# Kernel tuning notes

Measured on AMD Instinct MI355X. Metric: run time of the kernel, lower is better.

Reference implementation:

```python
import jax, jax.numpy as jnp
import numpy as np

N_DST = 100_000
N_SRC = 200_000
DEG = 16            # fixed avg degree -> E = N_DST*DEG
E = N_DST * DEG
P, K, W = 16, 256, 8  # num_parts, codebook entries, part width; feat_dim = P*W = 128
F_IN = P * W
F_OUT = 128


def setup_inputs() -> dict:
    key = jax.random.key(0)
    k1, k2, k3, k4, k5, k6, k7 = jax.random.split(key, 7)
    codes = jax.random.randint(k1, (N_SRC, P), 0, K, dtype=jnp.int32)
    indices = jax.random.randint(k2, (E,), 0, N_SRC, dtype=jnp.int32)
    indptr = (jnp.arange(N_DST + 1, dtype=jnp.int32) * DEG)
    h_self = jax.random.normal(k3, (N_DST, F_IN), dtype=jnp.float32)
    codebook = jax.random.normal(k4, (P, K, W), dtype=jnp.float32)
    W_neigh = jax.random.normal(k5, (F_OUT, F_IN), dtype=jnp.float32) * (1.0 / np.sqrt(F_IN))
    W_self = jax.random.normal(k6, (F_OUT, F_IN), dtype=jnp.float32) * (1.0 / np.sqrt(F_IN))
    b_self = jax.random.normal(k7, (F_OUT,), dtype=jnp.float32) * 0.01
    return {"codes": codes, "indices": indices, "indptr": indptr, "h_self": h_self,
            "codebook": codebook, "W_neigh": W_neigh, "W_self": W_self, "b_self": b_self}


def reference(codes, indices, indptr, h_self, codebook, W_neigh, W_self, b_self):
    n_dst = indptr.shape[0] - 1
    n_edges = indices.shape[0]
    # --- VQ decompress: codebook[p, codes[n, p]] -> [N_src, P, W] -> [N_src, F_IN]
    feat = codebook[jnp.arange(P)[None, :], codes]          # [N_src, P, W]
    feat = feat.reshape(feat.shape[0], F_IN)                # [N_src, F_IN]
    # --- CSR(CSC) mean SpMM over neighbors
    # dst id of each edge from indptr (jit-safe, static E)
    dst_ids = jnp.searchsorted(indptr, jnp.arange(n_edges, dtype=indptr.dtype), side="right") - 1
    gathered = feat[indices]                                 # [E, F_IN] (irregular gather)
    summed = jax.ops.segment_sum(gathered, dst_ids, num_segments=n_dst)  # [N_dst, F_IN]
    deg = jnp.diff(indptr).astype(summed.dtype)
    h_neigh = summed / jnp.maximum(deg, 1.0)[:, None]        # mean aggregation
    # --- linear combine: fc_neigh(h_neigh) + fc_self(h_self)
    rst = h_neigh @ W_neigh.T + h_self @ W_self.T + b_self[None, :]
    return rst
```

## Files before the change

### kernel.cpp

```cpp
#include <hip/hip_runtime.h>
#include <stdint.h>

constexpr int N_DST = 100000;
constexpr int N_SRC = 200000;
constexpr int DEG   = 16;
constexpr int PP    = 16;
constexpr int KK    = 256;
constexpr int WW    = 8;
constexpr int F_IN  = 128;
constexpr int F_OUT = 128;

typedef __attribute__((ext_vector_type(8))) short short8;
typedef __attribute__((ext_vector_type(4))) float floatx4;

__device__ __forceinline__ unsigned short f2bf(float f) {
    unsigned int u = __float_as_uint(f);
    unsigned int r = (u + 0x7FFFu + ((u >> 16) & 1u)) >> 16;
    return (unsigned short)r;
}
__device__ __forceinline__ float bf2f(unsigned int bits16) {
    return __uint_as_float(bits16 << 16);
}

constexpr int DT = 64;
constexpr int NT = (N_DST + DT - 1) / DT;
constexpr int LDS_STRIDE = 264;

__global__ __launch_bounds__(1024, 1) void fused_kernel(
    const int* __restrict__ codes, const int* __restrict__ indices,
    const float* __restrict__ codebook, const float* __restrict__ h_self,
    const float* __restrict__ Wn, const float* __restrict__ Ws,
    const float* __restrict__ b_self, float* __restrict__ out)
{
    __shared__ __align__(16) unsigned short scb[PP * KK * WW];
    __shared__ __align__(16) unsigned short hcat[DT][LDS_STRIDE];

    const int tid  = threadIdx.x;
    const int wv   = tid >> 6;
    const int lane = tid & 63;
    const int quad = lane >> 4;
    const int r    = lane & 15;
    const int p    = lane & 15;
    const int sub  = lane >> 4;

    {
        const float4* cb4 = (const float4*)codebook;
        ushort4* s4 = (ushort4*)scb;
        #pragma unroll
        for (int it = 0; it < 8; ++it) {
            const int i = tid + it * 1024;
            const float4 v = cb4[i];
            ushort4 w;
            w.x = f2bf(v.x); w.y = f2bf(v.y); w.z = f2bf(v.z); w.w = f2bf(v.w);
            s4[i] = w;
        }
    }

    const int cg = wv & 7;
    const int rg = wv >> 3;
    short8 bfrag[8];
    #pragma unroll
    for (int kt = 0; kt < 8; ++kt) {
        const int o  = cg * 16 + r;
        const int kb = kt * 32 + quad * 8;
        const float* src = (kb < 128) ? (Wn + o * 128 + kb)
                                      : (Ws + o * 128 + (kb - 128));
        union { short8 v; unsigned short u[8]; } f;
        #pragma unroll
        for (int j = 0; j < 8; ++j) f.u[j] = f2bf(src[j]);
        bfrag[kt] = f.v;
    }
    const float bs = b_self[cg * 16 + r];

    __syncthreads();

    for (int tile = blockIdx.x; tile < NT; tile += gridDim.x) {
        const int d0 = tile * DT;

        const int dbase = d0 + wv * 4;
        int sidx = 0;
        if (dbase + sub < N_DST) sidx = indices[dbase * DEG + lane];

        float4 hv[2];
        int hdl[2], hkq[2];
        #pragma unroll
        for (int it = 0; it < 2; ++it) {
            const int j  = tid + it * 1024;
            hdl[it] = j >> 5; hkq[it] = j & 31;
            const int d  = d0 + hdl[it];
            hv[it] = make_float4(0.f, 0.f, 0.f, 0.f);
            if (d < N_DST) hv[it] = ((const float4*)h_self)[(size_t)d * 32 + hkq[it]];
        }

        int c[16];
        #pragma unroll
        for (int e = 0; e < 16; ++e) {
            const int s = __shfl(sidx, (lane & 48) | e, 64);
            c[e] = codes[s * PP + p];
        }

        float ga[8];
        #pragma unroll
        for (int i = 0; i < 8; ++i) ga[i] = 0.f;
        #pragma unroll
        for (int e = 0; e < 16; ++e) {
            const uint4 q = *(const uint4*)(scb + (((p << 8) | c[e]) << 3));
            ga[0] += bf2f(q.x & 0xFFFFu);
            ga[1] += bf2f(q.x >> 16);
            ga[2] += bf2f(q.y & 0xFFFFu);
            ga[3] += bf2f(q.y >> 16);
            ga[4] += bf2f(q.z & 0xFFFFu);
            ga[5] += bf2f(q.z >> 16);
            ga[6] += bf2f(q.w & 0xFFFFu);
            ga[7] += bf2f(q.w >> 16);
        }

        {
            uint4 o4;
            o4.x = (unsigned int)f2bf(ga[0] * 0.0625f) | ((unsigned int)f2bf(ga[1] * 0.0625f) << 16);
            o4.y = (unsigned int)f2bf(ga[2] * 0.0625f) | ((unsigned int)f2bf(ga[3] * 0.0625f) << 16);
            o4.z = (unsigned int)f2bf(ga[4] * 0.0625f) | ((unsigned int)f2bf(ga[5] * 0.0625f) << 16);
            o4.w = (unsigned int)f2bf(ga[6] * 0.0625f) | ((unsigned int)f2bf(ga[7] * 0.0625f) << 16);
            *(uint4*)&hcat[wv * 4 + sub][p * 8] = o4;
        }
        #pragma unroll
        for (int it = 0; it < 2; ++it) {
            const unsigned int w0 = (unsigned int)f2bf(hv[it].x) | ((unsigned int)f2bf(hv[it].y) << 16);
            const unsigned int w1 = (unsigned int)f2bf(hv[it].z) | ((unsigned int)f2bf(hv[it].w) << 16);
            unsigned int* pr = (unsigned int*)&hcat[hdl[it]][128];
            pr[hkq[it] * 2]     = w0;
            pr[hkq[it] * 2 + 1] = w1;
        }
        __syncthreads();

        floatx4 acc[2];
        acc[0] = (floatx4)(0.f);
        acc[1] = (floatx4)(0.f);
        #pragma unroll
        for (int kt = 0; kt < 8; ++kt) {
            const short8 a0 = *(const short8*)&hcat[rg * 32 + r][kt * 32 + quad * 8];
            const short8 a1 = *(const short8*)&hcat[rg * 32 + 16 + r][kt * 32 + quad * 8];
            acc[0] = __builtin_amdgcn_mfma_f32_16x16x32_bf16(a0, bfrag[kt], acc[0], 0, 0, 0);
            acc[1] = __builtin_amdgcn_mfma_f32_16x16x32_bf16(a1, bfrag[kt], acc[1], 0, 0, 0);
        }

        #pragma unroll
        for (int m = 0; m < 2; ++m) {
            #pragma unroll
            for (int e = 0; e < 4; ++e) {
                const int d = d0 + rg * 32 + m * 16 + quad * 4 + e;
                if (d < N_DST) out[(size_t)d * F_OUT + cg * 16 + r] = acc[m][e] + bs;
            }
        }
        __syncthreads();
    }
}

extern "C" void kernel_launch(void* const* d_in, const int* in_sizes, int n_in,
                              void* d_out, int out_size, void* d_ws, size_t ws_size,
                              hipStream_t stream) {
    const int*   codes    = (const int*)d_in[0];
    const int*   indices  = (const int*)d_in[1];
    const float* h_self   = (const float*)d_in[3];
    const float* codebook = (const float*)d_in[4];
    const float* W_neigh  = (const float*)d_in[5];
    const float* W_self   = (const float*)d_in[6];
    const float* b_self   = (const float*)d_in[7];
    float*       out      = (float*)d_out;

    fused_kernel<<<256, 1024, 0, stream>>>(codes, indices, codebook, h_self,
                                           W_neigh, W_self, b_self, out);
}
```

Measured before the change: 163.3 us.

## Double-buffer LDS tiles to overlap next-tile gathers with MFMA and stores

```diff
diff --git a/kernel.cpp b/kernel.cpp
--- a/kernel.cpp
+++ b/kernel.cpp
@@ -10,6 +10,11 @@
 constexpr int F_IN  = 128;
 constexpr int F_OUT = 128;
 
+constexpr int DT = 64;
+constexpr int NT = (N_DST + DT - 1) / DT;
+constexpr int LDS_STRIDE = 264;
+constexpr int NBLK = 256;
+
 typedef __attribute__((ext_vector_type(8))) short short8;
 typedef __attribute__((ext_vector_type(4))) float floatx4;
 
@@ -22,9 +27,110 @@
     return __uint_as_float(bits16 << 16);
 }
 
-constexpr int DT = 64;
-constexpr int NT = (N_DST + DT - 1) / DT;
-constexpr int LDS_STRIDE = 264;
+__device__ __forceinline__ void gather_loads(
+    int d0, int tid, const int* __restrict__ indices,
+    const int* __restrict__ codes, const float* __restrict__ h_self,
+    int* c, float4* hv)
+{
+    const int lane = tid & 63;
+    const int wv   = tid >> 6;
+    const int p    = lane & 15;
+    const int sub  = lane >> 4;
+    const int d    = d0 + wv * 4 + sub;
+    const int dd   = (d < N_DST) ? d : (N_DST - 1);
+
+    int s[16];
+    #pragma unroll
+    for (int e = 0; e < 16; ++e) s[e] = indices[dd * DEG + e];
+
+    #pragma unroll
+    for (int it = 0; it < 2; ++it) {
+        const int j  = tid + it * 1024;
+        const int dl = j >> 5, kq = j & 31;
+        const int dh = d0 + dl;
+        hv[it] = make_float4(0.f, 0.f, 0.f, 0.f);
+        if (dh < N_DST) hv[it] = ((const float4*)h_self)[(size_t)dh * 32 + kq];
+    }
+
+    #pragma unroll
+    for (int e = 0; e < 16; ++e) c[e] = codes[s[e] * PP + p];
+}
+
+__device__ __forceinline__ void gather_finish(
+    int tid, const int* c, const float4* hv,
+    const unsigned short* __restrict__ scb,
+    unsigned short (*buf)[LDS_STRIDE])
+{
+    const int lane = tid & 63;
+    const int wv   = tid >> 6;
+    const int p    = lane & 15;
+    const int sub  = lane >> 4;
+
+    float ga[8];
+    #pragma unroll
+    for (int i = 0; i < 8; ++i) ga[i] = 0.f;
+    #pragma unroll
+    for (int e = 0; e < 16; ++e) {
+        const uint4 q = *(const uint4*)(scb + (((p << 8) | c[e]) << 3));
+        ga[0] += bf2f(q.x & 0xFFFFu);
+        ga[1] += bf2f(q.x >> 16);
+        ga[2] += bf2f(q.y & 0xFFFFu);
+        ga[3] += bf2f(q.y >> 16);
+        ga[4] += bf2f(q.z & 0xFFFFu);
+        ga[5] += bf2f(q.z >> 16);
+        ga[6] += bf2f(q.w & 0xFFFFu);
+        ga[7] += bf2f(q.w >> 16);
+    }
+
+    uint4 o4;
+    o4.x = (unsigned int)f2bf(ga[0] * 0.0625f) | ((unsigned int)f2bf(ga[1] * 0.0625f) << 16);
+    o4.y = (unsigned int)f2bf(ga[2] * 0.0625f) | ((unsigned int)f2bf(ga[3] * 0.0625f) << 16);
+    o4.z = (unsigned int)f2bf(ga[4] * 0.0625f) | ((unsigned int)f2bf(ga[5] * 0.0625f) << 16);
+    o4.w = (unsigned int)f2bf(ga[6] * 0.0625f) | ((unsigned int)f2bf(ga[7] * 0.0625f) << 16);
+    *(uint4*)&buf[wv * 4 + sub][p * 8] = o4;
+
+    #pragma unroll
+    for (int it = 0; it < 2; ++it) {
+        const int j  = tid + it * 1024;
+        const int dl = j >> 5, kq = j & 31;
+        uint2 w;
+        w.x = (unsigned int)f2bf(hv[it].x) | ((unsigned int)f2bf(hv[it].y) << 16);
+        w.y = (unsigned int)f2bf(hv[it].z) | ((unsigned int)f2bf(hv[it].w) << 16);
+        *(uint2*)&buf[dl][128 + kq * 4] = w;
+    }
+}
+
+__device__ __forceinline__ void mfma_store(
+    int d0, int tid, const short8* bfrag, float bs,
+    const unsigned short (*buf)[LDS_STRIDE], float* __restrict__ out)
+{
+    const int wv   = tid >> 6;
+    const int lane = tid & 63;
+    const int quad = lane >> 4;
+    const int r    = lane & 15;
+    const int cg   = wv & 7;
+    const int rg   = wv >> 3;
+
+    floatx4 acc0 = (floatx4)(0.f);
+    floatx4 acc1 = (floatx4)(0.f);
+    #pragma unroll
+    for (int kt = 0; kt < 8; ++kt) {
+        const short8 a0 = *(const short8*)&buf[rg * 32 + r][kt * 32 + quad * 8];
+        const short8 a1 = *(const short8*)&buf[rg * 32 + 16 + r][kt * 32 + quad * 8];
+        acc0 = __builtin_amdgcn_mfma_f32_16x16x32_bf16(a0, bfrag[kt], acc0, 0, 0, 0);
+        acc1 = __builtin_amdgcn_mfma_f32_16x16x32_bf16(a1, bfrag[kt], acc1, 0, 0, 0);
+    }
+    #pragma unroll
+    for (int e = 0; e < 4; ++e) {
+        const int da = d0 + rg * 32 + quad * 4 + e;
+        if (da < N_DST) out[(size_t)da * F_OUT + cg * 16 + r] = acc0[e] + bs;
+    }
+    #pragma unroll
+    for (int e = 0; e < 4; ++e) {
+        const int db = d0 + rg * 32 + 16 + quad * 4 + e;
+        if (db < N_DST) out[(size_t)db * F_OUT + cg * 16 + r] = acc1[e] + bs;
+    }
+}
 
 __global__ __launch_bounds__(1024, 1) void fused_kernel(
     const int* __restrict__ codes, const int* __restrict__ indices,
@@ -33,15 +139,13 @@
     const float* __restrict__ b_self, float* __restrict__ out)
 {
     __shared__ __align__(16) unsigned short scb[PP * KK * WW];
-    __shared__ __align__(16) unsigned short hcat[DT][LDS_STRIDE];
+    __shared__ __align__(16) unsigned short hcat[2][DT][LDS_STRIDE];
 
     const int tid  = threadIdx.x;
     const int wv   = tid >> 6;
     const int lane = tid & 63;
     const int quad = lane >> 4;
     const int r    = lane & 15;
-    const int p    = lane & 15;
-    const int sub  = lane >> 4;
 
     {
         const float4* cb4 = (const float4*)codebook;
@@ -57,7 +161,6 @@
     }
 
     const int cg = wv & 7;
-    const int rg = wv >> 3;
     short8 bfrag[8];
     #pragma unroll
     for (int kt = 0; kt < 8; ++kt) {
@@ -74,85 +177,26 @@
 
     __syncthreads();
 
-    for (int tile = blockIdx.x; tile < NT; tile += gridDim.x) {
-        const int d0 = tile * DT;
-
-        const int dbase = d0 + wv * 4;
-        int sidx = 0;
-        if (dbase + sub < N_DST) sidx = indices[dbase * DEG + lane];
-
-        float4 hv[2];
-        int hdl[2], hkq[2];
-        #pragma unroll
-        for (int it = 0; it < 2; ++it) {
-            const int j  = tid + it * 1024;
-            hdl[it] = j >> 5; hkq[it] = j & 31;
-            const int d  = d0 + hdl[it];
-            hv[it] = make_float4(0.f, 0.f, 0.f, 0.f);
-            if (d < N_DST) hv[it] = ((const float4*)h_self)[(size_t)d * 32 + hkq[it]];
-        }
-
-        int c[16];
-        #pragma unroll
-        for (int e = 0; e < 16; ++e) {
-            const int s = __shfl(sidx, (lane & 48) | e, 64);
-            c[e] = codes[s * PP + p];
-        }
-
-        float ga[8];
-        #pragma unroll
-        for (int i = 0; i < 8; ++i) ga[i] = 0.f;
-        #pragma unroll
-        for (int e = 0; e < 16; ++e) {
-            const uint4 q = *(const uint4*)(scb + (((p << 8) | c[e]) << 3));
-            ga[0] += bf2f(q.x & 0xFFFFu);
-            ga[1] += bf2f(q.x >> 16);
-            ga[2] += bf2f(q.y & 0xFFFFu);
-            ga[3] += bf2f(q.y >> 16);
-            ga[4] += bf2f(q.z & 0xFFFFu);
-            ga[5] += bf2f(q.z >> 16);
-            ga[6] += bf2f(q.w & 0xFFFFu);
-            ga[7] += bf2f(q.w >> 16);
-        }
-
-        {
-            uint4 o4;
-            o4.x = (unsigned int)f2bf(ga[0] * 0.0625f) | ((unsigned int)f2bf(ga[1] * 0.0625f) << 16);
-            o4.y = (unsigned int)f2bf(ga[2] * 0.0625f) | ((unsigned int)f2bf(ga[3] * 0.0625f) << 16);
-            o4.z = (unsigned int)f2bf(ga[4] * 0.0625f) | ((unsigned int)f2bf(ga[5] * 0.0625f) << 16);
-            o4.w = (unsigned int)f2bf(ga[6] * 0.0625f) | ((unsigned int)f2bf(ga[7] * 0.0625f) << 16);
-            *(uint4*)&hcat[wv * 4 + sub][p * 8] = o4;
-        }
-        #pragma unroll
-        for (int it = 0; it < 2; ++it) {
-            const unsigned int w0 = (unsigned int)f2bf(hv[it].x) | ((unsigned int)f2bf(hv[it].y) << 16);
-            const unsigned int w1 = (unsigned int)f2bf(hv[it].z) | ((unsigned int)f2bf(hv[it].w) << 16);
-            unsigned int* pr = (unsigned int*)&hcat[hdl[it]][128];
-            pr[hkq[it] * 2]     = w0;
-            pr[hkq[it] * 2 + 1] = w1;
-        }
+    const int t0 = (int)(((long long)blockIdx.x * NT) / NBLK);
+    const int t1 = (int)(((long long)(blockIdx.x + 1) * NT) / NBLK);
+
+    {
+        int c[16]; float4 hv[2];
+        gather_loads(t0 * DT, tid, indices, codes, h_self, c, hv);
+        gather_finish(tid, c, hv, scb, hcat[0]);
+    }
+
+    for (int t = t0; t < t1; ++t) {
+        const int cur = (t - t0) & 1;
         __syncthreads();
 
-        floatx4 acc[2];
-        acc[0] = (floatx4)(0.f);
-        acc[1] = (floatx4)(0.f);
-        #pragma unroll
-        for (int kt = 0; kt < 8; ++kt) {
-            const short8 a0 = *(const short8*)&hcat[rg * 32 + r][kt * 32 + quad * 8];
-            const short8 a1 = *(const short8*)&hcat[rg * 32 + 16 + r][kt * 32 + quad * 8];
-            acc[0] = __builtin_amdgcn_mfma_f32_16x16x32_bf16(a0, bfrag[kt], acc[0], 0, 0, 0);
-            acc[1] = __builtin_amdgcn_mfma_f32_16x16x32_bf16(a1, bfrag[kt], acc[1], 0, 0, 0);
-        }
-
-        #pragma unroll
-        for (int m = 0; m < 2; ++m) {
-            #pragma unroll
-            for (int e = 0; e < 4; ++e) {
-                const int d = d0 + rg * 32 + m * 16 + quad * 4 + e;
-                if (d < N_DST) out[(size_t)d * F_OUT + cg * 16 + r] = acc[m][e] + bs;
-            }
-        }
-        __syncthreads();
+        int c[16]; float4 hv[2];
+        const bool more = (t + 1 < t1);
+        if (more) gather_loads((t + 1) * DT, tid, indices, codes, h_self, c, hv);
+
+        mfma_store(t * DT, tid, bfrag, bs, hcat[cur], out);
+
+        if (more) gather_finish(tid, c, hv, scb, hcat[cur ^ 1]);
     }
 }
 
@@ -168,6 +212,6 @@
     const float* b_self   = (const float*)d_in[7];
     float*       out      = (float*)d_out;
 
-    fused_kernel<<<256, 1024, 0, stream>>>(codes, indices, codebook, h_self,
-                                           W_neigh, W_self, b_self, out);
-}
+    fused_kernel<<<NBLK, 1024, 0, stream>>>(codes, indices, codebook, h_self,
+                                            W_neigh, W_self, b_self, out);
+}
```

Result: no change. 165.8 us (+1.5%).
